# Performance work log

Hardware: AMD Instinct MI355X
Metric: run time of the kernel (lower is better)

The kernel has to match this reference:

```python
import jax, jax.numpy as jnp
import numpy as np

B, N, K = 8, 128, 8
N_HEADS, LATENT = 8, 128
D = N_HEADS * LATENT  # total_dim = 1024


def setup_inputs() -> dict:
    key = jax.random.key(0)
    ks = jax.random.split(key, 9)
    embedded = jax.random.normal(ks[0], (B, N, D), dtype=jnp.float32)
    # CoLight-style one-hot neighbor-selection adjacency: [B, N, K, N]
    nbr_idx = jax.random.randint(ks[1], (B, N, K), 0, N)
    adj_matrix = jax.nn.one_hot(nbr_idx, N, dtype=jnp.float32)
    s = 1.0 / np.sqrt(D)
    Wl = jax.random.uniform(ks[2], (D, D), jnp.float32, -s, s)
    bl = jax.random.uniform(ks[3], (D,), jnp.float32, -s, s)
    Wa = jax.random.uniform(ks[4], (D, D), jnp.float32, -s, s)
    ba = jax.random.uniform(ks[5], (D,), jnp.float32, -s, s)
    Wh = jax.random.uniform(ks[6], (D, D), jnp.float32, -s, s)
    bh = jax.random.uniform(ks[7], (D,), jnp.float32, -s, s)
    return {"embedded": embedded, "adj_matrix": adj_matrix,
            "Wl": Wl, "bl": bl, "Wa": Wa, "ba": ba, "Wh": Wh, "bh": bh}


def reference(embedded, adj_matrix, Wl, bl, Wa, ba, Wh, bh):
    b, n, d = embedded.shape
    H, L = N_HEADS, LATENT
    # torch: tile embedded to [B,N,N,D] then matmul with adj [B,N,K,N].
    # Equivalent without materializing the tile:
    neighbor_embed = jnp.einsum('bikn,bnd->bikd', adj_matrix, embedded)  # [B,N,K,D]

    agent = jax.nn.relu(embedded @ Wl + bl)                      # [B,N,D]
    # reshape (B,N,1,L,H) then permute (0,1,4,2,3) -> [B,N,H,1,L]
    agent_heads = agent.reshape(b, n, 1, L, H).transpose(0, 1, 4, 2, 3)

    nb = jax.nn.relu(neighbor_embed @ Wa + ba)
    neighbor_heads = nb.reshape(b, n, -1, L, H).transpose(0, 1, 4, 2, 3)  # [B,N,H,K,L]

    # einsum 'ijklm,ijknm->ijklm' with l=1: agent * sum over neighbors
    attn = agent_heads * neighbor_heads.sum(axis=3, keepdims=True)  # [B,N,H,1,L]
    attn = jax.nn.softmax(attn, axis=-1)

    nh = jax.nn.relu(neighbor_embed @ Wh + bh)
    neighbor_hidden = nh.reshape(b, n, -1, L, H).transpose(0, 1, 4, 2, 3)  # [B,N,H,K,L]

    out = attn * neighbor_hidden.sum(axis=3, keepdims=True)  # [B,N,H,1,L]
    out = out.mean(axis=2)                                   # [B,N,1,L]
    return out.reshape(b, n, -1)                             # [B,N,L]
```

## Files before the change

### kernel.cpp

```cpp
#include <hip/hip_runtime.h>
#include <math.h>

#define DD 1024
#define NN 128
#define BB 8
#define KNBR 8
#define NH 8
#define LL 128

typedef __attribute__((ext_vector_type(8))) short short8v;
typedef __attribute__((ext_vector_type(4))) float f32x4;

#define GLDS(gptr, lptr)                                                      \
  __builtin_amdgcn_global_load_lds(                                           \
      (const __attribute__((address_space(1))) void*)(gptr),                  \
      (__attribute__((address_space(3))) void*)(lptr), 16, 0, 0)

__device__ __forceinline__ unsigned short f2bf(float x) {
  unsigned u = __float_as_uint(x);
  unsigned r = u + 0x7fff + ((u >> 16) & 1);
  return (unsigned short)(r >> 16);
}
__device__ __forceinline__ float bf2f(unsigned short u) {
  return __uint_as_float((unsigned)u << 16);
}

__global__ __launch_bounds__(256)
void prep(const float* __restrict__ E,
          const float* __restrict__ Wl, const float* __restrict__ Wa,
          const float* __restrict__ Wh,
          unsigned short* __restrict__ Eb, unsigned short* __restrict__ Wt) {
  const int z = blockIdx.z;
  const int t = threadIdx.x;

  if (z == 3) {
    const int bid = blockIdx.y * 16 + blockIdx.x;
    const int i0 = bid * 4096 + t * 16;
    #pragma unroll
    for (int q = 0; q < 2; ++q) {
      const int i = i0 + q * 8;
      float4 a = *(const float4*)&E[i];
      float4 c = *(const float4*)&E[i + 4];
      union { unsigned short u[8]; uint4 v; } o;
      o.u[0] = f2bf(a.x); o.u[1] = f2bf(a.y); o.u[2] = f2bf(a.z); o.u[3] = f2bf(a.w);
      o.u[4] = f2bf(c.x); o.u[5] = f2bf(c.y); o.u[6] = f2bf(c.z); o.u[7] = f2bf(c.w);
      *(uint4*)&Eb[i] = o.v;
    }
    return;
  }

  const float* W = (z == 0) ? Wl : (z == 1) ? Wa : Wh;
  unsigned short* out = Wt + (size_t)z * DD * DD;

  __shared__ unsigned short tile[64][65];
  const int tx = t & 15, ty = t >> 4;
  const int r0 = blockIdx.y * 64, c0 = blockIdx.x * 64;

  #pragma unroll
  for (int i = 0; i < 4; ++i) {
    const int r = ty + i * 16;
    float4 v = *(const float4*)&W[(size_t)(r0 + r) * DD + c0 + tx * 4];
    tile[r][tx * 4 + 0] = f2bf(v.x);
    tile[r][tx * 4 + 1] = f2bf(v.y);
    tile[r][tx * 4 + 2] = f2bf(v.z);
    tile[r][tx * 4 + 3] = f2bf(v.w);
  }
  __syncthreads();
  #pragma unroll
  for (int i = 0; i < 4; ++i) {
    const int rr = ty + i * 16;
    ushort4 o;
    o.x = tile[tx * 4 + 0][rr];
    o.y = tile[tx * 4 + 1][rr];
    o.z = tile[tx * 4 + 2][rr];
    o.w = tile[tx * 4 + 3][rr];
    *(ushort4*)&out[(size_t)(c0 + rr) * DD + r0 + tx * 4] = o;
  }
}

__global__ __launch_bounds__(256)
void gemm3_mfma(const unsigned short* __restrict__ Eb,
                const unsigned short* __restrict__ Wt,
                const float* __restrict__ bl, const float* __restrict__ ba,
                const float* __restrict__ bh,
                unsigned short* __restrict__ Ylb,
                unsigned short* __restrict__ Yab,
                unsigned short* __restrict__ Yhb) {
  const int orig = blockIdx.x;
  const int job = (orig & 7) * 96 + (orig >> 3);
  const int mat = job >> 8;
  const int rem = job & 255;
  const int bx = rem >> 4;
  const int by = rem & 15;

  const unsigned short* Bg = Wt + (size_t)mat * DD * DD;
  const float* bias = (mat == 0) ? bl : (mat == 1) ? ba : bh;

  __shared__ unsigned short As[3][64 * 64];
  __shared__ unsigned short Bs[3][64 * 64];

  const int t = threadIdx.x;
  const int lane = t & 63;
  const int w = t >> 6;
  const int wr = w >> 1, wc = w & 1;
  const int brow = by * 64, bcol = bx * 64;

  const int srow = t >> 3;
  const int sk = (((t & 7) ^ (srow & 7)) * 8);
  const unsigned short* gA = Eb + (size_t)(brow + srow) * DD + sk;
  const unsigned short* gB = Bg + (size_t)(bcol + srow) * DD + sk;
  const int ldsoff = w * 512;

  const int lrow = lane & 15, lg = lane >> 4;

  int aidx[2][2], bidx[2][2];
  #pragma unroll
  for (int kk = 0; kk < 2; ++kk)
    #pragma unroll
    for (int m = 0; m < 2; ++m) {
      const int ra = wr * 32 + m * 16 + lrow;
      aidx[kk][m] = ra * 64 + (((kk * 4 + lg) ^ (ra & 7)) * 8);
      const int rb = wc * 32 + m * 16 + lrow;
      bidx[kk][m] = rb * 64 + (((kk * 4 + lg) ^ (rb & 7)) * 8);
    }

  float bv0 = bias[bcol + wc * 32 + lrow];
  float bv1 = bias[bcol + wc * 32 + 16 + lrow];
  asm volatile("" : "+v"(bv0), "+v"(bv1));

  f32x4 acc[2][2] = {};

#define STAGE(q, kt) do {                                                     \
    const int k0_ = (kt) * 64;                                                \
    GLDS(gA + k0_,           &As[q][ldsoff]);                                 \
    GLDS(gA + k0_ + 32 * DD, &As[q][2048 + ldsoff]);                          \
    GLDS(gB + k0_,           &Bs[q][ldsoff]);                                 \
    GLDS(gB + k0_ + 32 * DD, &Bs[q][2048 + ldsoff]);                          \
  } while (0)

  STAGE(0, 0);
  STAGE(1, 1);

  #pragma unroll
  for (int kt = 0; kt < 16; ++kt) {
    const int p = kt % 3;
    if (kt != 15) asm volatile("s_waitcnt vmcnt(4)" ::: "memory");
    else          asm volatile("s_waitcnt vmcnt(0)" ::: "memory");
    __builtin_amdgcn_s_barrier();
    if (kt + 2 < 16) STAGE((kt + 2) % 3, kt + 2);

    short8v a[2][2], b[2][2];
    #pragma unroll
    for (int kk = 0; kk < 2; ++kk)
      #pragma unroll
      for (int m = 0; m < 2; ++m) {
        a[kk][m] = *(const short8v*)&As[p][aidx[kk][m]];
        b[kk][m] = *(const short8v*)&Bs[p][bidx[kk][m]];
      }

    __builtin_amdgcn_s_setprio(1);
    #pragma unroll
    for (int kk = 0; kk < 2; ++kk)
      #pragma unroll
      for (int m = 0; m < 2; ++m)
        #pragma unroll
        for (int n = 0; n < 2; ++n)
          acc[m][n] = __builtin_amdgcn_mfma_f32_16x16x32_bf16(
              a[kk][m], b[kk][n], acc[m][n], 0, 0, 0);
    __builtin_amdgcn_s_setprio(0);
  }
#undef STAGE

  unsigned short* Yo = (mat == 0) ? Ylb : (mat == 1) ? Yab : Yhb;
  #pragma unroll
  for (int m = 0; m < 2; ++m) {
    #pragma unroll
    for (int n = 0; n < 2; ++n) {
      const int col = bcol + wc * 32 + n * 16 + lrow;
      const int r0  = brow + wr * 32 + m * 16 + lg * 4;
      const float bv = n ? bv1 : bv0;
      #pragma unroll
      for (int j = 0; j < 4; ++j)
        Yo[(size_t)(r0 + j) * DD + col] = f2bf(fmaxf(acc[m][n][j] + bv, 0.f));
    }
  }
}

__global__ __launch_bounds__(256)
void colight_epilogue(const float* __restrict__ adj,
                      const unsigned short* __restrict__ Ylb,
                      const unsigned short* __restrict__ Yab,
                      const unsigned short* __restrict__ Yhb,
                      float* __restrict__ out) {
  const int bid = blockIdx.x;
  const int bi = (bid & 7) * NN + (bid >> 3);
  const int b  = bi >> 7;

  __shared__ int   idxs[KNBR];
  __shared__ float sA[NH][LL];
  __shared__ float sH[NH][LL];
  __shared__ float sL[NH][LL];
  __shared__ float sPart[NH][LL];

  const int t = threadIdx.x;

  const float* arow = adj + (size_t)bi * KNBR * NN;
  {
    const int k = t >> 5, j = t & 31;
    float4 v = *(const float4*)&arow[k * NN + j * 4];
    const int base = j * 4;
    if (v.x > 0.5f) idxs[k] = base;
    if (v.y > 0.5f) idxs[k] = base + 1;
    if (v.z > 0.5f) idxs[k] = base + 2;
    if (v.w > 0.5f) idxs[k] = base + 3;
  }
  __syncthreads();

  const int rbase = b * NN;
  int ridx[KNBR];
  #pragma unroll
  for (int k = 0; k < KNBR; ++k) ridx[k] = rbase + idxs[k];

  const int d0 = t * 4;
  const int gl = t >> 1;
  const int h0 = (t & 1) * 4;
  {
    float a0 = 0.f, a1 = 0.f, a2 = 0.f, a3 = 0.f;
    float g0 = 0.f, g1 = 0.f, g2 = 0.f, g3 = 0.f;
    #pragma unroll
    for (int k = 0; k < KNBR; ++k) {
      const size_t rr = (size_t)ridx[k] * DD + d0;
      ushort4 va = *(const ushort4*)&Yab[rr];
      ushort4 vh = *(const ushort4*)&Yhb[rr];
      a0 += bf2f(va.x); a1 += bf2f(va.y); a2 += bf2f(va.z); a3 += bf2f(va.w);
      g0 += bf2f(vh.x); g1 += bf2f(vh.y); g2 += bf2f(vh.z); g3 += bf2f(vh.w);
    }
    ushort4 vl = *(const ushort4*)&Ylb[(size_t)bi * DD + d0];
    sA[h0 + 0][gl] = a0; sA[h0 + 1][gl] = a1;
    sA[h0 + 2][gl] = a2; sA[h0 + 3][gl] = a3;
    sH[h0 + 0][gl] = g0; sH[h0 + 1][gl] = g1;
    sH[h0 + 2][gl] = g2; sH[h0 + 3][gl] = g3;
    sL[h0 + 0][gl] = bf2f(vl.x); sL[h0 + 1][gl] = bf2f(vl.y);
    sL[h0 + 2][gl] = bf2f(vl.z); sL[h0 + 3][gl] = bf2f(vl.w);
  }
  __syncthreads();

  const int h = t >> 5, j = t & 31;
  float z[4];
  float mx = -1e30f;
  #pragma unroll
  for (int q = 0; q < 4; ++q) {
    const int l = j + q * 32;
    z[q] = sL[h][l] * sA[h][l];
    mx = fmaxf(mx, z[q]);
  }
  #pragma unroll
  for (int m = 1; m <= 16; m <<= 1)
    mx = fmaxf(mx, __shfl_xor(mx, m, 32));

  float se = 0.f;
  #pragma unroll
  for (int q = 0; q < 4; ++q) {
    z[q] = __expf(z[q] - mx);
    se += z[q];
  }
  #pragma unroll
  for (int m = 1; m <= 16; m <<= 1)
    se += __shfl_xor(se, m, 32);
  const float inv = 1.f / se;

  #pragma unroll
  for (int q = 0; q < 4; ++q) {
    const int l = j + q * 32;
    sPart[h][l] = z[q] * inv * sH[h][l] * 0.125f;
  }
  __syncthreads();

  if (t < LL) {
    float o = 0.f;
    #pragma unroll
    for (int hh = 0; hh < NH; ++hh) o += sPart[hh][t];
    out[(size_t)bi * LL + t] = o;
  }
}

extern "C" void kernel_launch(void* const* d_in, const int* in_sizes, int n_in,
                              void* d_out, int out_size, void* d_ws, size_t ws_size,
                              hipStream_t stream) {
  const float* E   = (const float*)d_in[0];
  const float* adj = (const float*)d_in[1];
  const float* Wl  = (const float*)d_in[2];
  const float* bl  = (const float*)d_in[3];
  const float* Wa  = (const float*)d_in[4];
  const float* ba  = (const float*)d_in[5];
  const float* Wh  = (const float*)d_in[6];
  const float* bh  = (const float*)d_in[7];
  float* out = (float*)d_out;

  char* ws = (char*)d_ws;
  unsigned short* Ylb = (unsigned short*)ws;
  unsigned short* Yab = (unsigned short*)(ws + 2 * 1024 * 1024);
  unsigned short* Yhb = (unsigned short*)(ws + 4 * 1024 * 1024);
  unsigned short* Eb  = (unsigned short*)(ws + 6 * 1024 * 1024);
  unsigned short* Wt  = (unsigned short*)(ws + 8 * 1024 * 1024);

  prep<<<dim3(16, 16, 4), dim3(256), 0, stream>>>(E, Wl, Wa, Wh, Eb, Wt);
  gemm3_mfma<<<dim3(768), dim3(256), 0, stream>>>(Eb, Wt, bl, ba, bh,
                                                  Ylb, Yab, Yhb);
  colight_epilogue<<<dim3(BB * NN), dim3(256), 0, stream>>>(adj, Ylb, Yab, Yhb, out);
}
```

Before: 27.91 us.

## Fuse three GEMMs per block sharing the A tile across weight matrices

The GEMM kernel now has each 512-thread block compute the same 64x64 output tile for all three weight matrices, so the activation tile is loaded once and reused across Wl, Wa and Wh. Grid shrinks from 768 to 256 blocks, the K-step drops to 32 with a 4-deep LDS ring buffer, and eight waves split the loads. This cuts redundant A-tile traffic. The cost is fewer blocks, which may underfill the GPU's CUs, more barriers per block, and more LDS per block.

```diff
diff --git a/kernel.cpp b/kernel.cpp
--- a/kernel.cpp
+++ b/kernel.cpp
@@ -78,7 +78,7 @@
   }
 }
 
-__global__ __launch_bounds__(256)
+__global__ __launch_bounds__(512)
 void gemm3_mfma(const unsigned short* __restrict__ Eb,
                 const unsigned short* __restrict__ Wt,
                 const float* __restrict__ bl, const float* __restrict__ ba,
@@ -87,101 +87,102 @@
                 unsigned short* __restrict__ Yab,
                 unsigned short* __restrict__ Yhb) {
   const int orig = blockIdx.x;
-  const int job = (orig & 7) * 96 + (orig >> 3);
-  const int mat = job >> 8;
-  const int rem = job & 255;
-  const int bx = rem >> 4;
-  const int by = rem & 15;
-
-  const unsigned short* Bg = Wt + (size_t)mat * DD * DD;
-  const float* bias = (mat == 0) ? bl : (mat == 1) ? ba : bh;
-
-  __shared__ unsigned short As[3][64 * 64];
-  __shared__ unsigned short Bs[3][64 * 64];
+  const int job = (orig & 7) * 32 + (orig >> 3);
+  const int bx = job >> 4;
+  const int by = job & 15;
+
+  __shared__ unsigned short As[4][2048];
+  __shared__ unsigned short Bs[4][3][2048];
 
   const int t = threadIdx.x;
   const int lane = t & 63;
   const int w = t >> 6;
-  const int wr = w >> 1, wc = w & 1;
+  const int wr = w >> 2, wc = w & 3;
   const int brow = by * 64, bcol = bx * 64;
 
-  const int srow = t >> 3;
-  const int sk = (((t & 7) ^ (srow & 7)) * 8);
-  const unsigned short* gA = Eb + (size_t)(brow + srow) * DD + sk;
-  const unsigned short* gB = Bg + (size_t)(bcol + srow) * DD + sk;
-  const int ldsoff = w * 512;
+  const int prow = lane >> 2;
+  const int schunk = (lane & 3) ^ ((lane >> 3) & 3);
+  const int qq = w & 3;
+  const unsigned short* Wt0 = Wt;
+  const unsigned short* Wt1 = Wt + (size_t)DD * DD;
+  const unsigned short* Wt2 = Wt + 2 * (size_t)DD * DD;
+  const unsigned short* s0 = (w < 4)
+      ? Eb  + (size_t)(brow + qq * 16 + prow) * DD + schunk * 8
+      : Wt0 + (size_t)(bcol + qq * 16 + prow) * DD + schunk * 8;
+  const unsigned short* s1 = (w < 4)
+      ? Wt1 + (size_t)(bcol + qq * 16 + prow) * DD + schunk * 8
+      : Wt2 + (size_t)(bcol + qq * 16 + prow) * DD + schunk * 8;
+  const int qoff = qq * 512;
 
   const int lrow = lane & 15, lg = lane >> 4;
-
-  int aidx[2][2], bidx[2][2];
-  #pragma unroll
-  for (int kk = 0; kk < 2; ++kk)
-    #pragma unroll
-    for (int m = 0; m < 2; ++m) {
-      const int ra = wr * 32 + m * 16 + lrow;
-      aidx[kk][m] = ra * 64 + (((kk * 4 + lg) ^ (ra & 7)) * 8);
-      const int rb = wc * 32 + m * 16 + lrow;
-      bidx[kk][m] = rb * 64 + (((kk * 4 + lg) ^ (rb & 7)) * 8);
-    }
-
-  float bv0 = bias[bcol + wc * 32 + lrow];
-  float bv1 = bias[bcol + wc * 32 + 16 + lrow];
-  asm volatile("" : "+v"(bv0), "+v"(bv1));
-
-  f32x4 acc[2][2] = {};
-
-#define STAGE(q, kt) do {                                                     \
-    const int k0_ = (kt) * 64;                                                \
-    GLDS(gA + k0_,           &As[q][ldsoff]);                                 \
-    GLDS(gA + k0_ + 32 * DD, &As[q][2048 + ldsoff]);                          \
-    GLDS(gB + k0_,           &Bs[q][ldsoff]);                                 \
-    GLDS(gB + k0_ + 32 * DD, &Bs[q][2048 + ldsoff]);                          \
+  int aoff[2], boff[3];
+  #pragma unroll
+  for (int m = 0; m < 2; ++m) {
+    const int ra = wr * 32 + m * 16 + lrow;
+    aoff[m] = ra * 32 + (lg ^ ((ra >> 1) & 3)) * 8;
+  }
+  {
+    const int rb = wc * 16 + lrow;
+    const int bo = rb * 32 + (lg ^ ((rb >> 1) & 3)) * 8;
+    boff[0] = bo; boff[1] = bo; boff[2] = bo;
+  }
+
+  float bv[3];
+  bv[0] = bl[bcol + wc * 16 + lrow];
+  bv[1] = ba[bcol + wc * 16 + lrow];
+  bv[2] = bh[bcol + wc * 16 + lrow];
+  asm volatile("" : "+v"(bv[0]), "+v"(bv[1]), "+v"(bv[2]));
+
+  f32x4 acc[3][2] = {};
+
+#define STAGE(p, kt) do {                                                     \
+    GLDS(s0 + (kt) * 32, ((w < 4) ? &As[p][0] : &Bs[p][0][0]) + qoff);        \
+    GLDS(s1 + (kt) * 32, &Bs[p][(w < 4) ? 1 : 2][0] + qoff);                  \
   } while (0)
 
   STAGE(0, 0);
   STAGE(1, 1);
-
-  #pragma unroll
-  for (int kt = 0; kt < 16; ++kt) {
-    const int p = kt % 3;
-    if (kt != 15) asm volatile("s_waitcnt vmcnt(4)" ::: "memory");
-    else          asm volatile("s_waitcnt vmcnt(0)" ::: "memory");
+  STAGE(2, 2);
+
+  #pragma unroll
+  for (int kt = 0; kt < 32; ++kt) {
+    const int p = kt & 3;
+    if (kt < 30)       asm volatile("s_waitcnt vmcnt(4)" ::: "memory");
+    else if (kt == 30) asm volatile("s_waitcnt vmcnt(2)" ::: "memory");
+    else               asm volatile("s_waitcnt vmcnt(0)" ::: "memory");
     __builtin_amdgcn_s_barrier();
-    if (kt + 2 < 16) STAGE((kt + 2) % 3, kt + 2);
-
-    short8v a[2][2], b[2][2];
-    #pragma unroll
-    for (int kk = 0; kk < 2; ++kk)
-      #pragma unroll
-      for (int m = 0; m < 2; ++m) {
-        a[kk][m] = *(const short8v*)&As[p][aidx[kk][m]];
-        b[kk][m] = *(const short8v*)&Bs[p][bidx[kk][m]];
-      }
+    if (kt + 3 < 32) STAGE((kt + 3) & 3, kt + 3);
+
+    short8v av[2], bvv[3];
+    #pragma unroll
+    for (int m = 0; m < 2; ++m)
+      av[m] = *(const short8v*)&As[p][aoff[m]];
+    #pragma unroll
+    for (int mat = 0; mat < 3; ++mat)
+      bvv[mat] = *(const short8v*)&Bs[p][mat][boff[mat]];
 
     __builtin_amdgcn_s_setprio(1);
     #pragma unroll
-    for (int kk = 0; kk < 2; ++kk)
+    for (int mat = 0; mat < 3; ++mat)
       #pragma unroll
       for (int m = 0; m < 2; ++m)
-        #pragma unroll
-        for (int n = 0; n < 2; ++n)
-          acc[m][n] = __builtin_amdgcn_mfma_f32_16x16x32_bf16(
-              a[kk][m], b[kk][n], acc[m][n], 0, 0, 0);
+        acc[mat][m] = __builtin_amdgcn_mfma_f32_16x16x32_bf16(
+            av[m], bvv[mat], acc[mat][m], 0, 0, 0);
     __builtin_amdgcn_s_setprio(0);
   }
 #undef STAGE
 
-  unsigned short* Yo = (mat == 0) ? Ylb : (mat == 1) ? Yab : Yhb;
-  #pragma unroll
-  for (int m = 0; m < 2; ++m) {
-    #pragma unroll
-    for (int n = 0; n < 2; ++n) {
-      const int col = bcol + wc * 32 + n * 16 + lrow;
-      const int r0  = brow + wr * 32 + m * 16 + lg * 4;
-      const float bv = n ? bv1 : bv0;
+  const int col = bcol + wc * 16 + lrow;
+  #pragma unroll
+  for (int mat = 0; mat < 3; ++mat) {
+    unsigned short* Yo = (mat == 0) ? Ylb : (mat == 1) ? Yab : Yhb;
+    #pragma unroll
+    for (int m = 0; m < 2; ++m) {
+      const int r0 = brow + wr * 32 + m * 16 + lg * 4;
       #pragma unroll
       for (int j = 0; j < 4; ++j)
-        Yo[(size_t)(r0 + j) * DD + col] = f2bf(fmaxf(acc[m][n][j] + bv, 0.f));
+        Yo[(size_t)(r0 + j) * DD + col] =
+            f2bf(fmaxf(acc[mat][m][j] + bv[mat], 0.f));
     }
   }
 }
@@ -305,7 +306,7 @@
   unsigned short* Wt  = (unsigned short*)(ws + 8 * 1024 * 1024);
 
   prep<<<dim3(16, 16, 4), dim3(256), 0, stream>>>(E, Wl, Wa, Wh, Eb, Wt);
-  gemm3_mfma<<<dim3(768), dim3(256), 0, stream>>>(Eb, Wt, bl, ba, bh,
+  gemm3_mfma<<<dim3(256), dim3(512), 0, stream>>>(Eb, Wt, bl, ba, bh,
                                                   Ylb, Yab, Yhb);
   colight_epilogue<<<dim3(BB * NN), dim3(256), 0, stream>>>(adj, Ylb, Yab, Yhb, out);
 }
```

New measurement: 32.06 us. 14.9% more time.
